# Optimization experiments

Hardware: AMD Instinct MI355X
Metric: run time of the kernel (lower is better)

The kernel has to match this reference:

```python
import jax, jax.numpy as jnp
import numpy as np
import math

B, S, H = 2, 2048, 1024
NH, HD = 16, 64
EPS = 1e-12


def setup_inputs() -> dict:
    key = jax.random.key(0)
    ks = jax.random.split(key, 6)
    scale = 1.0 / math.sqrt(H)
    return {
        "hidden_states": jax.random.normal(ks[0], (B, S, H), jnp.float32),
        "Wq": jax.random.normal(ks[1], (H, H), jnp.float32) * scale,
        "bq": jnp.zeros((H,), jnp.float32),
        "Wk": jax.random.normal(ks[2], (H, H), jnp.float32) * scale,
        "bk": jnp.zeros((H,), jnp.float32),
        "Wv": jax.random.normal(ks[3], (H, H), jnp.float32) * scale,
        "bv": jnp.zeros((H,), jnp.float32),
        "Wo": jax.random.normal(ks[4], (H, H), jnp.float32) * scale,
        "bo": jnp.zeros((H,), jnp.float32),
        "gamma": jnp.ones((H,), jnp.float32),
        "beta": jnp.zeros((H,), jnp.float32),
    }


def _heads(x):
    # [B, S, H] -> [B, NH, S, HD]
    return x.reshape(B, S, NH, HD).transpose(0, 2, 1, 3)


def reference(hidden_states, Wq, bq, Wk, bk, Wv, bv, Wo, bo, gamma, beta):
    q = _heads(hidden_states @ Wq + bq)
    k = _heads(hidden_states @ Wk + bk)
    v = _heads(hidden_states @ Wv + bv)
    # scores: [B, NH, S, S]
    scores = jnp.einsum("bhqd,bhkd->bhqk", q, k) / math.sqrt(HD)
    probs = jax.nn.softmax(scores, axis=-1)
    ctx = jnp.einsum("bhqk,bhkd->bhqd", probs, v)
    ctx = ctx.transpose(0, 2, 1, 3).reshape(B, S, H)
    attn_out = ctx @ Wo + bo
    x = attn_out + hidden_states
    mu = jnp.mean(x, axis=-1, keepdims=True)
    var = jnp.var(x, axis=-1, keepdims=True)
    return (x - mu) / jnp.sqrt(var + EPS) * gamma + beta
```

## Files before the change

### kernel.cpp

```cpp
#include <hip/hip_runtime.h>
#include <hip/hip_bf16.h>

#define B_ 2
#define S_ 2048
#define H_ 1024
#define NH_ 16
#define HD_ 64
#define M_ (B_*S_)

typedef __attribute__((ext_vector_type(8))) short bf16x8;
typedef __attribute__((ext_vector_type(4))) short bf16x4;
typedef __attribute__((ext_vector_type(4))) float f32x4;
typedef __attribute__((ext_vector_type(4))) int   i32x4;

__device__ inline float waveReduceSum(float v) {
#pragma unroll
  for (int off = 32; off >= 1; off >>= 1) v += __shfl_xor(v, off);
  return v;
}

__device__ inline short f2bf(float f) {
  union { float f; unsigned u; } v; v.f = f;
  unsigned r = v.u + 0x7fffu + ((v.u >> 16) & 1u);
  return (short)(r >> 16);
}

__device__ inline unsigned cvt_pk_bf16(float lo, float hi) {
  unsigned w;
  asm("v_cvt_pk_bf16_f32 %0, %1, %2" : "=v"(w) : "v"(lo), "v"(hi));
  return w;
}

__device__ inline void async_load16(const void* g, void* l) {
  __builtin_amdgcn_global_load_lds(
      (const __attribute__((address_space(1))) void*)g,
      (__attribute__((address_space(3))) void*)l, 16, 0, 0);
}

__device__ inline int swz8(int r) { return (r & 3) | (((r >> 3) & 1) << 2); }

__global__ __launch_bounds__(256)
void cvt_bf16(const float* __restrict__ in, short* __restrict__ out) {
  const size_t i = (size_t)blockIdx.x * 256 + threadIdx.x;
  float4 v = ((const float4*)in)[i];
  bf16x4 o;
  o[0] = f2bf(v.x); o[1] = f2bf(v.y); o[2] = f2bf(v.z); o[3] = f2bf(v.w);
  ((bf16x4*)out)[i] = o;
}

__global__ __launch_bounds__(256)
void transpose_w4(const float* __restrict__ W0, const float* __restrict__ W1,
                  const float* __restrict__ W2, const float* __restrict__ W3,
                  short* __restrict__ Tqkv, short* __restrict__ To) {
  const float* W; short* T;
  switch (blockIdx.z) {
    case 0: W = W0; T = Tqkv; break;
    case 1: W = W1; T = Tqkv + (size_t)1024 * 1024; break;
    case 2: W = W2; T = Tqkv + (size_t)2048 * 1024; break;
    default: W = W3; T = To; break;
  }
  __shared__ float tile[32][36];
  const int tid = threadIdx.x;
  const int tx = tid & 7, ty = tid >> 3;
  const int k0 = blockIdx.y << 5, n0 = blockIdx.x << 5;
  float4 v = *(const float4*)&W[(size_t)(k0 + ty) * H_ + n0 + (tx << 2)];
  tile[ty][(tx << 2) + 0] = v.x;
  tile[ty][(tx << 2) + 1] = v.y;
  tile[ty][(tx << 2) + 2] = v.z;
  tile[ty][(tx << 2) + 3] = v.w;
  __syncthreads();
  bf16x4 o;
  o[0] = f2bf(tile[(tx << 2) + 0][ty]);
  o[1] = f2bf(tile[(tx << 2) + 1][ty]);
  o[2] = f2bf(tile[(tx << 2) + 2][ty]);
  o[3] = f2bf(tile[(tx << 2) + 3][ty]);
  *(bf16x4*)&T[(size_t)(n0 + ty) * H_ + k0 + (tx << 2)] = o;
}

#define QKV_NT 32

__global__ __launch_bounds__(512)
void gemm_qkv(const short* __restrict__ A, const short* __restrict__ Bt,
              const float* __restrict__ bq, const float* __restrict__ bk,
              const float* __restrict__ bv, short* __restrict__ Qo,
              short* __restrict__ Ko, short* __restrict__ Vto) {
  __shared__ short A_lds[2][256][32];
  __shared__ short B_lds[2][256][32];
  const int tid = threadIdx.x;
  const int lane = tid & 63, wv = tid >> 6;
  const int l16 = lane & 15, lg = lane >> 4;
  const int wr = wv >> 2, wc = wv & 3;
  const int swzb = (blockIdx.x & 7) * 24 + (blockIdx.x >> 3);
  const int bx = swzb % 12, by = swzb / 12;
  const int m0 = by << 8, n0 = bx << 8;
  const int K = H_;

  const int srow = lane >> 2;
  const int sch  = lane & 3;

#define QKV_STAGE(buf, t_)                                                     \
  {                                                                            \
    const int k0_ = (t_) << 5;                                                 \
    _Pragma("unroll")                                                          \
    for (int i_ = 0; i_ < 2; ++i_) {                                           \
      const int r0_ = 128 * i_ + 16 * wv;                                      \
      async_load16(A + (size_t)(m0 + r0_ + srow) * K + k0_ + (sch << 3),       \
                   &A_lds[buf][r0_][0]);                                       \
      async_load16(Bt + (size_t)(n0 + r0_ + srow) * K + k0_ + (sch << 3),      \
                   &B_lds[buf][r0_][0]);                                       \
    }                                                                          \
  }

  f32x4 acc[8][4] = {};

  QKV_STAGE(0, 0)
  QKV_STAGE(1, 1)
  asm volatile("s_waitcnt vmcnt(4)" ::: "memory");
  __builtin_amdgcn_s_barrier();
  __builtin_amdgcn_sched_barrier(0);

  for (int t = 0; t < QKV_NT; ++t) {
    const int cur = t & 1;
    bf16x8 af[8], bfr[4];
#pragma unroll
    for (int i = 0; i < 8; ++i)
      af[i] = *(const bf16x8*)&A_lds[cur][128 * wr + 16 * i + l16][8 * lg];
#pragma unroll
    for (int j = 0; j < 4; ++j)
      bfr[j] = *(const bf16x8*)&B_lds[cur][64 * wc + 16 * j + l16][8 * lg];
    __builtin_amdgcn_s_setprio(1);
#pragma unroll
    for (int i = 0; i < 8; ++i)
#pragma unroll
      for (int j = 0; j < 4; ++j)
        acc[i][j] = __builtin_amdgcn_mfma_f32_16x16x32_bf16(af[i], bfr[j], acc[i][j], 0, 0, 0);
    __builtin_amdgcn_s_setprio(0);
    __builtin_amdgcn_sched_barrier(0);
    __builtin_amdgcn_s_barrier();
    __builtin_amdgcn_sched_barrier(0);
    if (t + 2 < QKV_NT) {
      QKV_STAGE(cur, t + 2)
      asm volatile("s_waitcnt vmcnt(4)" ::: "memory");
    } else {
      asm volatile("s_waitcnt vmcnt(0)" ::: "memory");
    }
    __builtin_amdgcn_s_barrier();
    __builtin_amdgcn_sched_barrier(0);
  }
#undef QKV_STAGE

  const int mt = n0 >> 10;
  const float* bias = (mt == 0) ? bq : (mt == 1 ? bk : bv);
  const float qs = (mt == 0) ? 0.125f * 1.4426950408889634f : 1.0f;

  if (mt < 2) {
    short* Out = (mt == 0) ? Qo : Ko;
#pragma unroll
    for (int i = 0; i < 8; ++i) {
#pragma unroll
      for (int j = 0; j < 4; ++j) {
        const int nl = (n0 & 1023) + 64 * wc + 16 * j + l16;
        const float bvl = bias[nl];
        const int h = nl >> 6, d = nl & 63;
#pragma unroll
        for (int r = 0; r < 4; ++r) {
          const int m = m0 + 128 * wr + 16 * i + 4 * lg + r;
          const int b = m >> 11, s = m & (S_ - 1);
          Out[(((size_t)(b * NH_ + h) * S_ + s) << 6) + d] =
              f2bf((acc[i][j][r] + bvl) * qs);
        }
      }
    }
  } else {
#pragma unroll
    for (int i = 0; i < 8; ++i) {
      const int mb = m0 + 128 * wr + 16 * i + 4 * lg;
      const int b = mb >> 11, s = mb & (S_ - 1);
#pragma unroll
      for (int j = 0; j < 4; ++j) {
        const int nl = (n0 & 1023) + 64 * wc + 16 * j + l16;
        const float bvl = bias[nl];
        const int h = nl >> 6, d = nl & 63;
        bf16x4 pk;
#pragma unroll
        for (int r = 0; r < 4; ++r) pk[r] = f2bf(acc[i][j][r] + bvl);
        *(bf16x4*)&Vto[(((size_t)(b * NH_ + h) * HD_ + d) << 11) + s] = pk;
      }
    }
  }
}

__global__ __launch_bounds__(256)
void gemm_o(const short* __restrict__ A, const short* __restrict__ Bt,
            const float* __restrict__ bias, float* __restrict__ C) {
  __shared__ short A_lds[2][64][32];
  __shared__ short B_lds[2][128][32];
  const int tid = threadIdx.x;
  const int lane = tid & 63, wv = tid >> 6;
  const int l16 = lane & 15, lg = lane >> 4;
  const int wr = wv >> 1, wc = wv & 1;
  const int swzb = (blockIdx.x & 7) * 64 + (blockIdx.x >> 3);
  const int bx = swzb & 7, by = swzb >> 3;
  const int m0 = by << 6, n0 = bx << 7;
  const int K = H_;

  const int srow = lane >> 2, soff = (lane & 3) << 3;

  f32x4 acc[2][4] = {};

  async_load16(A + (size_t)(m0 + 16 * wv + srow) * K + soff, &A_lds[0][16 * wv][0]);
#pragma unroll
  for (int i = 0; i < 2; ++i) {
    const int c = 2 * wv + i;
    async_load16(Bt + (size_t)(n0 + 16 * c + srow) * K + soff, &B_lds[0][16 * c][0]);
  }

  int cur = 0;
  for (int t = 0; t < K / 32; ++t) {
    __syncthreads();
    if (t + 1 < K / 32) {
      const int k0 = (t + 1) << 5;
      async_load16(A + (size_t)(m0 + 16 * wv + srow) * K + k0 + soff,
                   &A_lds[cur ^ 1][16 * wv][0]);
#pragma unroll
      for (int i = 0; i < 2; ++i) {
        const int c = 2 * wv + i;
        async_load16(Bt + (size_t)(n0 + 16 * c + srow) * K + k0 + soff,
                     &B_lds[cur ^ 1][16 * c][0]);
      }
    }
    bf16x8 af[2], bfr[4];
#pragma unroll
    for (int i = 0; i < 2; ++i)
      af[i] = *(const bf16x8*)&A_lds[cur][32 * wr + 16 * i + l16][8 * lg];
#pragma unroll
    for (int j = 0; j < 4; ++j)
      bfr[j] = *(const bf16x8*)&B_lds[cur][64 * wc + 16 * j + l16][8 * lg];
#pragma unroll
    for (int i = 0; i < 2; ++i)
#pragma unroll
      for (int j = 0; j < 4; ++j)
        acc[i][j] = __builtin_amdgcn_mfma_f32_16x16x32_bf16(af[i], bfr[j], acc[i][j], 0, 0, 0);
    cur ^= 1;
  }

#pragma unroll
  for (int i = 0; i < 2; ++i)
#pragma unroll
    for (int j = 0; j < 4; ++j) {
      const int n = n0 + 64 * wc + 16 * j + l16;
      const float bvl = bias[n];
#pragma unroll
      for (int r = 0; r < 4; ++r) {
        const int m = m0 + 32 * wr + 16 * i + 4 * lg + r;
        C[(size_t)m * H_ + n] = acc[i][j][r] + bvl;
      }
    }
}

__global__ __launch_bounds__(256)
void attn_mfma(const short* __restrict__ Qg, const short* __restrict__ Kg,
               const short* __restrict__ Vtg, short* __restrict__ ctxb) {
  __shared__ short K_lds[2][2][64][64];
  __shared__ short V_t[2][2][64][64];

  const int tid  = threadIdx.x;
  const int lane = tid & 63;
  const int wv   = tid >> 6;
  const int l16  = lane & 15, lg = lane >> 4;

  const int swz = (blockIdx.x & 7) * 128 + (blockIdx.x >> 3);
  const int bh = swz >> 5, qb = swz & 31;

  const short* Qh = Qg + ((size_t)bh * S_ << 6);
  const short* Kh = Kg + ((size_t)bh * S_ << 6);
  const short* Vh = Vtg + ((size_t)bh << 6) * S_;

  const int q0 = qb * 64 + wv * 16;

  bf16x8 qf[2];
  qf[0] = *(const bf16x8*)&Qh[((size_t)(q0 + l16) << 6) + 8 * lg];
  qf[1] = *(const bf16x8*)&Qh[((size_t)(q0 + l16) << 6) + 8 * lg + 32];

  const int l16part = ((l16 >> 2) << 3) + (l16 & 3);

  const int kr = tid >> 2;
  const int cb = (tid & 3) << 1;
  const int sz = swz8(kr);
  const int c1 = ((cb    ) ^ sz) << 3;
  const int c2 = ((cb + 1) ^ sz) << 3;

  f32x4 o[4] = {};
  float m_run = -1e30f, l_run = 0.f;

#pragma unroll
  for (int h = 0; h < 2; ++h) {
    const size_t kg = ((size_t)(64 * h + kr)) << 6;
    *(bf16x8*)&K_lds[0][h][kr][c1] = *(const bf16x8*)&Kh[kg + (cb << 3)];
    *(bf16x8*)&K_lds[0][h][kr][c2] = *(const bf16x8*)&Kh[kg + ((cb + 1) << 3)];
    const size_t vg = (size_t)kr * S_ + 64 * h;
    *(bf16x8*)&V_t[0][h][kr][c1]   = *(const bf16x8*)&Vh[vg + (cb << 3)];
    *(bf16x8*)&V_t[0][h][kr][c2]   = *(const bf16x8*)&Vh[vg + ((cb + 1) << 3)];
  }

  int cur = 0;
  for (int t = 0; t < S_ / 128; ++t) {
    bf16x8 nk[2][2], nv[2][2];
    const bool pre = (t + 1 < S_ / 128);
    if (pre) {
      const int kvn = (t + 1) * 128;
#pragma unroll
      for (int h = 0; h < 2; ++h) {
        const size_t kb = ((size_t)(kvn + 64 * h + kr)) << 6;
        nk[h][0] = *(const bf16x8*)&Kh[kb + (cb << 3)];
        nk[h][1] = *(const bf16x8*)&Kh[kb + ((cb + 1) << 3)];
        const size_t vb = (size_t)kr * S_ + kvn + 64 * h;
        nv[h][0] = *(const bf16x8*)&Vh[vb + (cb << 3)];
        nv[h][1] = *(const bf16x8*)&Vh[vb + ((cb + 1) << 3)];
      }
    }
    __syncthreads();

    f32x4 s[2][4] = {};
    __builtin_amdgcn_s_setprio(1);
#pragma unroll
    for (int h = 0; h < 2; ++h)
#pragma unroll
      for (int ks = 0; ks < 2; ++ks)
#pragma unroll
        for (int tt = 0; tt < 4; ++tt) {
          const int krow = ((tt >> 1) << 5) + ((tt & 1) << 2) + l16part;
          const int kch = (lg + 4 * ks) ^ swz8(krow);
          bf16x8 kf = *(const bf16x8*)&K_lds[cur][h][krow][kch << 3];
          s[h][tt] = __builtin_amdgcn_mfma_f32_16x16x32_bf16(kf, qf[ks], s[h][tt], 0, 0, 0);
        }
    __builtin_amdgcn_s_setprio(0);

    float pmax = -1e30f;
#pragma unroll
    for (int h = 0; h < 2; ++h)
#pragma unroll
      for (int tt = 0; tt < 4; ++tt)
        pmax = fmaxf(pmax, fmaxf(fmaxf(s[h][tt][0], s[h][tt][1]),
                                 fmaxf(s[h][tt][2], s[h][tt][3])));
    pmax = fmaxf(pmax, __shfl_xor(pmax, 16));
    pmax = fmaxf(pmax, __shfl_xor(pmax, 32));

    float p[2][4][4];
    float rs = 0.f;
    if (__any(pmax - m_run > 8.0f)) {
      const float mn = fmaxf(m_run, pmax);
      const float scl = __builtin_amdgcn_exp2f(m_run - mn);
      m_run = mn;
#pragma unroll
      for (int h = 0; h < 2; ++h)
#pragma unroll
        for (int tt = 0; tt < 4; ++tt)
#pragma unroll
          for (int r = 0; r < 4; ++r) {
            p[h][tt][r] = __builtin_amdgcn_exp2f(s[h][tt][r] - mn);
            rs += p[h][tt][r];
          }
      rs += __shfl_xor(rs, 16);
      rs += __shfl_xor(rs, 32);
      l_run = l_run * scl + rs;
      float sclr[4];
#pragma unroll
      for (int r = 0; r < 4; ++r) sclr[r] = __shfl(scl, 4 * lg + r);
#pragma unroll
      for (int tt = 0; tt < 4; ++tt)
#pragma unroll
        for (int r = 0; r < 4; ++r) o[tt][r] *= sclr[r];
    } else {
#pragma unroll
      for (int h = 0; h < 2; ++h)
#pragma unroll
        for (int tt = 0; tt < 4; ++tt)
#pragma unroll
          for (int r = 0; r < 4; ++r) {
            p[h][tt][r] = __builtin_amdgcn_exp2f(s[h][tt][r] - m_run);
            rs += p[h][tt][r];
          }
      rs += __shfl_xor(rs, 16);
      rs += __shfl_xor(rs, 32);
      l_run += rs;
    }

    unsigned w[2][4][2];
#pragma unroll
    for (int h = 0; h < 2; ++h)
#pragma unroll
      for (int tt = 0; tt < 4; ++tt) {
        w[h][tt][0] = cvt_pk_bf16(p[h][tt][0], p[h][tt][1]);
        w[h][tt][1] = cvt_pk_bf16(p[h][tt][2], p[h][tt][3]);
      }

    __builtin_amdgcn_s_setprio(1);
#pragma unroll
    for (int h = 0; h < 2; ++h)
#pragma unroll
      for (int ks = 0; ks < 2; ++ks) {
        i32x4 aw;
        aw[0] = (int)w[h][2 * ks][0];
        aw[1] = (int)w[h][2 * ks][1];
        aw[2] = (int)w[h][2 * ks + 1][0];
        aw[3] = (int)w[h][2 * ks + 1][1];
        const bf16x8 pf = __builtin_bit_cast(bf16x8, aw);
#pragma unroll
        for (int tt = 0; tt < 4; ++tt) {
          const int vrow = 16 * tt + l16;
          const int vch = (lg + 4 * ks) ^ swz8(vrow);
          bf16x8 vf = *(const bf16x8*)&V_t[cur][h][vrow][vch << 3];
          o[tt] = __builtin_amdgcn_mfma_f32_16x16x32_bf16(pf, vf, o[tt], 0, 0, 0);
        }
      }
    __builtin_amdgcn_s_setprio(0);

    if (pre) {
#pragma unroll
      for (int h = 0; h < 2; ++h) {
        *(bf16x8*)&K_lds[cur ^ 1][h][kr][c1] = nk[h][0];
        *(bf16x8*)&K_lds[cur ^ 1][h][kr][c2] = nk[h][1];
        *(bf16x8*)&V_t[cur ^ 1][h][kr][c1]   = nv[h][0];
        *(bf16x8*)&V_t[cur ^ 1][h][kr][c2]   = nv[h][1];
      }
    }
    cur ^= 1;
  }

  float invr[4];
#pragma unroll
  for (int r = 0; r < 4; ++r) invr[r] = 1.f / __shfl(l_run, 4 * lg + r);
  const int b = bh >> 4, h = bh & 15;
#pragma unroll
  for (int r = 0; r < 4; ++r) {
    const int q = q0 + 4 * lg + r;
#pragma unroll
    for (int tt = 0; tt < 4; ++tt)
      ctxb[(((size_t)(b * S_ + q) * NH_ + h) << 6) + 16 * tt + l16] =
          f2bf(o[tt][r] * invr[r]);
  }
}

__global__ __launch_bounds__(256)
void resid_ln(const float* __restrict__ attn_out, const float* __restrict__ hs,
              const float* __restrict__ gamma, const float* __restrict__ beta,
              float* __restrict__ out) {
  __shared__ float reds[4], reds2[4];
  const int row = blockIdx.x;
  const int tid = threadIdx.x;
  const float4* a4 = (const float4*)(attn_out + ((size_t)row << 10));
  const float4* h4 = (const float4*)(hs + ((size_t)row << 10));
  float4 a = a4[tid], h = h4[tid];
  float e0 = a.x + h.x, e1 = a.y + h.y, e2 = a.z + h.z, e3 = a.w + h.w;
  float s  = e0 + e1 + e2 + e3;
  float sq = e0 * e0 + e1 * e1 + e2 * e2 + e3 * e3;
  s = waveReduceSum(s);
  sq = waveReduceSum(sq);
  const int lane = tid & 63, wave = tid >> 6;
  if (lane == 0) { reds[wave] = s; reds2[wave] = sq; }
  __syncthreads();
  const float S1 = reds[0] + reds[1] + reds[2] + reds[3];
  const float S2 = reds2[0] + reds2[1] + reds2[2] + reds2[3];
  const float mu = S1 * (1.f / H_);
  const float var = S2 * (1.f / H_) - mu * mu;
  const float rstd = rsqrtf(var + 1e-12f);
  const float4 g = ((const float4*)gamma)[tid];
  const float4 bb = ((const float4*)beta)[tid];
  float4 o;
  o.x = (e0 - mu) * rstd * g.x + bb.x;
  o.y = (e1 - mu) * rstd * g.y + bb.y;
  o.z = (e2 - mu) * rstd * g.z + bb.z;
  o.w = (e3 - mu) * rstd * g.w + bb.w;
  ((float4*)(out + ((size_t)row << 10)))[tid] = o;
}

extern "C" void kernel_launch(void* const* d_in, const int* in_sizes, int n_in,
                              void* d_out, int out_size, void* d_ws, size_t ws_size,
                              hipStream_t stream) {
  const float* X     = (const float*)d_in[0];
  const float* Wq    = (const float*)d_in[1];
  const float* bq    = (const float*)d_in[2];
  const float* Wk    = (const float*)d_in[3];
  const float* bk    = (const float*)d_in[4];
  const float* Wv    = (const float*)d_in[5];
  const float* bv    = (const float*)d_in[6];
  const float* Wo    = (const float*)d_in[7];
  const float* bo    = (const float*)d_in[8];
  const float* gamma = (const float*)d_in[9];
  const float* beta  = (const float*)d_in[10];
  float* out = (float*)d_out;

  char* ws = (char*)d_ws;
  short* Xbf  = (short*)ws;
  short* Wqkv = (short*)(ws + ( 8u << 20));
  short* Wto  = (short*)(ws + (14u << 20));
  short* Qbf  = (short*)(ws + (16u << 20));
  short* Kbf  = (short*)(ws + (24u << 20));
  short* Vt   = (short*)(ws + (32u << 20));
  short* ctxb = Xbf;
  float* attn = (float*)(ws + (16u << 20));

  dim3 blk(256);
  hipLaunchKernelGGL(cvt_bf16, dim3((M_ * H_) / 1024), blk, 0, stream, X, Xbf);
  hipLaunchKernelGGL(transpose_w4, dim3(32, 32, 4), blk, 0, stream,
                     Wq, Wk, Wv, Wo, Wqkv, Wto);
  hipLaunchKernelGGL(gemm_qkv, dim3(192), dim3(512), 0, stream,
                     Xbf, Wqkv, bq, bk, bv, Qbf, Kbf, Vt);
  hipLaunchKernelGGL(attn_mfma, dim3(1024), blk, 0, stream, Qbf, Kbf, Vt, ctxb);
  hipLaunchKernelGGL(gemm_o, dim3(512), blk, 0, stream, ctxb, Wto, bo, attn);
  hipLaunchKernelGGL(resid_ln, dim3(M_), blk, 0, stream, attn, X, gamma, beta, out);
}
```

Before: 237.7 us.

## Stream K/V tiles into LDS with async direct-to-LDS loads in attention

The attention kernel's K and V^T double-buffered prefetch no longer passes through registers and explicit LDS stores. Each wave now issues async 16-byte global-to-LDS loads into the next buffer at the top of each iteration. A vmcnt(0) wait plus barrier at the end of the iteration replaces the old __syncthreads and the trailing register-to-LDS writes. The aim is to cut VGPR pressure and ds_write instructions and to overlap the loads with the MFMA work. The cost is that every iteration waits for all outstanding loads before its barrier, and correctness depends on the async_load16 helper and the per-lane swizzled chunk addressing matching the reader layout.

```diff
diff --git a/kernel.cpp b/kernel.cpp
--- a/kernel.cpp
+++ b/kernel.cpp
@@ -284,42 +284,36 @@
 
   const int l16part = ((l16 >> 2) << 3) + (l16 & 3);
 
-  const int kr = tid >> 2;
-  const int cb = (tid & 3) << 1;
-  const int sz = swz8(kr);
-  const int c1 = ((cb    ) ^ sz) << 3;
-  const int c2 = ((cb + 1) ^ sz) << 3;
+  const int srow8 = lane >> 3;
+  const int schk  = lane & 7;
 
   f32x4 o[4] = {};
   float m_run = -1e30f, l_run = 0.f;
 
-#pragma unroll
-  for (int h = 0; h < 2; ++h) {
-    const size_t kg = ((size_t)(64 * h + kr)) << 6;
-    *(bf16x8*)&K_lds[0][h][kr][c1] = *(const bf16x8*)&Kh[kg + (cb << 3)];
-    *(bf16x8*)&K_lds[0][h][kr][c2] = *(const bf16x8*)&Kh[kg + ((cb + 1) << 3)];
-    const size_t vg = (size_t)kr * S_ + 64 * h;
-    *(bf16x8*)&V_t[0][h][kr][c1]   = *(const bf16x8*)&Vh[vg + (cb << 3)];
-    *(bf16x8*)&V_t[0][h][kr][c2]   = *(const bf16x8*)&Vh[vg + ((cb + 1) << 3)];
-  }
-
-  int cur = 0;
+#define ASTAGE(buf, kv0)                                                       \
+  {                                                                            \
+    _Pragma("unroll")                                                          \
+    for (int h_ = 0; h_ < 2; ++h_) {                                           \
+      _Pragma("unroll")                                                        \
+      for (int i_ = 0; i_ < 2; ++i_) {                                         \
+        const int row_ = 16 * wv + 8 * i_ + srow8;                             \
+        const int ch_ = schk ^ swz8(row_);                                     \
+        async_load16(Kh + (((size_t)((kv0) + 64 * h_ + row_)) << 6) + (ch_ << 3), \
+                     &K_lds[buf][h_][16 * wv + 8 * i_][0]);                    \
+        async_load16(Vh + (size_t)row_ * S_ + (kv0) + 64 * h_ + (ch_ << 3),    \
+                     &V_t[buf][h_][16 * wv + 8 * i_][0]);                      \
+      }                                                                        \
+    }                                                                          \
+  }
+
+  ASTAGE(0, 0)
+  asm volatile("s_waitcnt vmcnt(0)" ::: "memory");
+  __builtin_amdgcn_s_barrier();
+  __builtin_amdgcn_sched_barrier(0);
+
   for (int t = 0; t < S_ / 128; ++t) {
-    bf16x8 nk[2][2], nv[2][2];
-    const bool pre = (t + 1 < S_ / 128);
-    if (pre) {
-      const int kvn = (t + 1) * 128;
-#pragma unroll
-      for (int h = 0; h < 2; ++h) {
-        const size_t kb = ((size_t)(kvn + 64 * h + kr)) << 6;
-        nk[h][0] = *(const bf16x8*)&Kh[kb + (cb << 3)];
-        nk[h][1] = *(const bf16x8*)&Kh[kb + ((cb + 1) << 3)];
-        const size_t vb = (size_t)kr * S_ + kvn + 64 * h;
-        nv[h][0] = *(const bf16x8*)&Vh[vb + (cb << 3)];
-        nv[h][1] = *(const bf16x8*)&Vh[vb + ((cb + 1) << 3)];
-      }
-    }
-    __syncthreads();
+    const int cur = t & 1;
+    if (t + 1 < S_ / 128) ASTAGE(cur ^ 1, (t + 1) * 128)
 
     f32x4 s[2][4] = {};
     __builtin_amdgcn_s_setprio(1);
@@ -416,17 +410,11 @@
       }
     __builtin_amdgcn_s_setprio(0);
 
-    if (pre) {
-#pragma unroll
-      for (int h = 0; h < 2; ++h) {
-        *(bf16x8*)&K_lds[cur ^ 1][h][kr][c1] = nk[h][0];
-        *(bf16x8*)&K_lds[cur ^ 1][h][kr][c2] = nk[h][1];
-        *(bf16x8*)&V_t[cur ^ 1][h][kr][c1]   = nv[h][0];
-        *(bf16x8*)&V_t[cur ^ 1][h][kr][c2]   = nv[h][1];
-      }
-    }
-    cur ^= 1;
-  }
+    asm volatile("s_waitcnt vmcnt(0)" ::: "memory");
+    __builtin_amdgcn_s_barrier();
+    __builtin_amdgcn_sched_barrier(0);
+  }
+#undef ASTAGE
 
   float invr[4];
 #pragma unroll
```

Measured after the change: 241.9 us. Within noise of the previous version (+1.8%).
